# Kernel tuning notes

Hardware: AMD Instinct MI355X
Metric: run time of the kernel (lower is better)

Reference implementation:

```python
import jax, jax.numpy as jnp
import numpy as np

C = 768; H = 12; D = C // H; R = 8; SCALE = 0.5; EPS = 1e-12
NEG = -1e9

def _lin(x, W, b):
    return x @ W + b

def _ln(x, g, b):
    m = jnp.mean(x, axis=-1, keepdims=True)
    v = jnp.mean((x - m) ** 2, axis=-1, keepdims=True)
    return (x - m) * jax.lax.rsqrt(v + EPS) * g + b

def setup_inputs() -> dict:
    key = jax.random.key(0)
    ks = jax.random.split(key, 16)
    B, T, K = 8, 512, 4
    s = 0.02
    inp = {
        'x': jax.random.normal(ks[0], (B, T, C), jnp.float32),
        'mask': jnp.ones((B, T), jnp.int32),
        'neighbour_rep': jax.random.normal(ks[1], (B, T - 1, K, C), jnp.float32),
        'Wq': jax.random.normal(ks[2], (C, C), jnp.float32) * s,
        'bq': jnp.zeros((C,), jnp.float32),
        'Wk': jax.random.normal(ks[3], (C, C), jnp.float32) * s,
        'bk': jnp.zeros((C,), jnp.float32),
        'Wv': jax.random.normal(ks[4], (C, C), jnp.float32) * s,
        'bv': jnp.zeros((C,), jnp.float32),
        'Wp': jax.random.normal(ks[5], (C, C), jnp.float32) * s,
        'bp': jnp.zeros((C,), jnp.float32),
        'Wd': jax.random.normal(ks[6], (C, R), jnp.float32) * s,
        'bd': jnp.zeros((R,), jnp.float32),
        'Wu': jax.random.normal(ks[7], (R, C), jnp.float32) * s,
        'bu': jnp.zeros((C,), jnp.float32),
        'ln_g': jnp.ones((C,), jnp.float32),
        'ln_b': jnp.zeros((C,), jnp.float32),
    }
    return inp

def _softmax_stable(att):
    # manual max-sub-exp-sum softmax, matching stable_softmax
    att = att - jnp.max(att, axis=-1, keepdims=True)
    att = jnp.exp(att)
    return att / jnp.sum(att, axis=-1, keepdims=True)

def _heads(t, n_tok):
    B = t.shape[0]
    return t.reshape(B, n_tok, H, D)

def reference(x, mask, neighbour_rep, Wq, bq, Wk, bk, Wv, bv, Wp, bp, Wd, bd, Wu, bu, ln_g, ln_b):
    B, T, _ = x.shape
    inv = 1.0 / jnp.sqrt(jnp.float32(D))
    mvalid = (mask != 0)[:, None, None, :]  # [B,1,1,T]

    # ---- self attention: queries are x[:,1:], keys/values over full seq ----
    q = _heads(_lin(x[:, 1:], Wq, bq), T - 1)      # [B,T-1,H,D]
    k = _heads(_lin(x, Wk, bk), T)                 # [B,T,H,D]
    v = _heads(_lin(x, Wv, bv), T)
    att = jnp.einsum('bqhd,bkhd->bhqk', q, k) * inv
    att = jnp.where(mvalid, att, NEG)
    att = _softmax_stable(att)
    y_self = jnp.einsum('bhqk,bkhd->bqhd', att, v).reshape(B, T - 1, C)
    y_self = _lin(y_self, Wp, bp)

    # ---- cls attention: single query (token 0), low-rank key projection ----
    qc = _heads(_lin(x[:, :1], Wq, bq), 1)                         # [B,1,H,D]
    kc = _heads(_lin(_lin(x, Wd, bd), Wu, bu), T)                  # [B,T,H,D]
    attc = jnp.einsum('bqhd,bkhd->bhqk', qc, kc) * inv
    attc = jnp.where(mvalid, attc, NEG)
    attc = _softmax_stable(attc)
    y_cls = jnp.einsum('bhqk,bkhd->bqhd', attc, v).reshape(B, 1, C)
    y_cls = _lin(y_cls, Wp, bp)

    # ---- neighbour attention over small candidate set per token ----
    cand = jnp.concatenate([x[:, 1:, None, :], neighbour_rep], axis=2)  # [B,T-1,Kc,C]
    Kc = cand.shape[2]
    qn = _lin(cand, Wq, bq).reshape(B, T - 1, Kc, H, D)
    kn = _lin(_lin(cand, Wd, bd), Wu, bu).reshape(B, T - 1, Kc, H, D)
    vn = _lin(cand, Wv, bv).reshape(B, T - 1, Kc, H, D)
    attn = jnp.einsum('btihd,btjhd->bthij', qn, kn) * inv
    attn = _softmax_stable(attn)
    out = jnp.einsum('bthij,btjhd->btihd', attn, vn).reshape(B, T - 1, Kc, C)
    out = _lin(out, Wp, bp)
    y_neigh = out[:, :, 0, :]
    neigh_tmp = out[:, :, 1:, :]

    y = SCALE * y_neigh + (1.0 - SCALE) * y_self
    neighbour_out = _ln(neigh_tmp + neighbour_rep, ln_g, ln_b)
    y = jnp.concatenate([y_cls, y], axis=1)
    y = _ln(y + x, ln_g, ln_b)
    return y, neighbour_out
```

## Files before the change

kernel.cpp:

```cpp
#include <hip/hip_runtime.h>
#include <math.h>

#define C_    768
#define H_    12
#define D_    64
#define B_    8
#define T_    512
#define TM1   511
#define R_    8
#define KN_   4
#define KC5   5
#define SCALE_ 0.5f
#define EPS_  1e-12f
#define NEG_  -1000000000.0f
#define INV_  0.125f
#define LDQ   2560
#define QPOFF 2304
#define NT_   4096
#define NRR_  16352

typedef __bf16 bf16_t;
typedef __bf16 bf16x4_t __attribute__((ext_vector_type(4)));
typedef __bf16 bf16x8_t __attribute__((ext_vector_type(8)));
typedef float  f32x4_t  __attribute__((ext_vector_type(4)));
typedef const void __attribute__((address_space(1)))* gas_t;
typedef void       __attribute__((address_space(3)))* las_t;

__device__ __forceinline__ void gl_lds16(const bf16_t* g, bf16_t* l) {
  __builtin_amdgcn_global_load_lds((gas_t)g, (las_t)l, 16, 0, 0);
}

struct GemmDesc {
  const bf16_t* A; int lda;
  const bf16_t* Bt;
  const float* bias;
  bf16_t* Cbf; int ldc;
  bf16_t* Ctr; int trcol0; int mode;
  int M, K, N, gx, nwg;
};

__global__ __launch_bounds__(256) void prep(
    const float* __restrict__ x, const float* __restrict__ nrep,
    const float* __restrict__ Wq, const float* __restrict__ Wk,
    const float* __restrict__ Wv, const float* __restrict__ Wp,
    const float* __restrict__ Wd, const float* __restrict__ Wu,
    const float* __restrict__ bq, const float* __restrict__ bk,
    const float* __restrict__ bv, const float* __restrict__ bu,
    const float* __restrict__ bp,
    bf16_t* __restrict__ xbf, bf16_t* __restrict__ nrbf,
    bf16_t* __restrict__ Wbig, bf16_t* __restrict__ Wtp,
    bf16_t* __restrict__ Wvbf,
    float* __restrict__ WdT, float* __restrict__ bbig,
    float* __restrict__ zb768)
{
  __shared__ float tile[32][33];
  const int bid = blockIdx.x, tid = threadIdx.x;
  if (bid < 1024) {
    const long n = (long)NT_ * C_;
    for (long i = ((long)bid * 256 + tid) * 4; i < n; i += (long)1024 * 256 * 4) {
      float4 v = *(const float4*)(x + i);
      bf16x4_t o = {(bf16_t)v.x, (bf16_t)v.y, (bf16_t)v.z, (bf16_t)v.w};
      *(bf16x4_t*)(xbf + i) = o;
    }
  } else if (bid < 3072) {
    const long n = (long)NRR_ * C_;
    for (long i = ((long)(bid - 1024) * 256 + tid) * 4; i < n;
         i += (long)2048 * 256 * 4) {
      float4 v = *(const float4*)(nrep + i);
      bf16x4_t o = {(bf16_t)v.x, (bf16_t)v.y, (bf16_t)v.z, (bf16_t)v.w};
      *(bf16x4_t*)(nrbf + i) = o;
    }
  } else if (bid < 5376) {
    int sub = bid - 3072;
    const int which = sub / 576; sub %= 576;
    if (which == 2) {
      const long i = ((long)sub * 256 + tid) * 4;
      float4 v = *(const float4*)(Wv + i);
      bf16x4_t o = {(bf16_t)v.x, (bf16_t)v.y, (bf16_t)v.z, (bf16_t)v.w};
      *(bf16x4_t*)(Wvbf + i) = o;
    } else {
      const float* W = which == 0 ? Wq : which == 1 ? Wk : Wp;
      bf16_t* Wt = (which == 3) ? Wtp : Wbig + (size_t)which * C_ * C_;
      const int n0 = (sub % 24) * 32, k0 = (sub / 24) * 32;
      const int tx = tid & 31, ty = tid >> 5;
      #pragma unroll
      for (int r = ty; r < 32; r += 8)
        tile[r][tx] = W[(size_t)(k0 + r) * C_ + n0 + tx];
      __syncthreads();
      #pragma unroll
      for (int r = ty; r < 32; r += 8)
        Wt[(size_t)(n0 + r) * C_ + k0 + tx] = (bf16_t)tile[tx][r];
    }
  } else if (bid < 6144) {
    const int idx = (bid - 5376) * 256 + tid;
    const int n = idx / C_, k = idx % C_;
    const int h = n >> 4, r = n & 15;
    float s = 0.f;
    if (h < H_) {
      if (r < 8) {
        #pragma unroll 8
        for (int j = 0; j < 64; ++j)
          s += Wu[r * C_ + h * 64 + j] * Wq[(size_t)k * C_ + h * 64 + j];
      } else if (r == 8) {
        #pragma unroll 8
        for (int j = 0; j < 64; ++j)
          s += bu[h * 64 + j] * Wq[(size_t)k * C_ + h * 64 + j];
      }
    }
    Wbig[(size_t)(QPOFF + n) * C_ + k] = (bf16_t)s;
  } else if (bid < 6168) {
    const int idx = (bid - 6144) * 256 + tid;
    if (idx < R_ * C_) {
      const int r = idx / C_, k = idx % C_;
      WdT[idx] = Wd[(size_t)k * R_ + r];
    }
  } else {
    const int i = (bid - 6168) * 256 + tid;
    if (i < 2560) {
      float v;
      if (i < 768) v = bq[i];
      else if (i < 1536) v = bk[i - 768];
      else if (i < 2304) {
        const int n = i - 1536;
        float s = bp[n];
        for (int m = 0; m < C_; ++m) s += bv[m] * Wp[(size_t)m * C_ + n];
        v = s;
      } else {
        const int n = i - 2304, h = n >> 4, r = n & 15;
        v = 0.f;
        if (h < H_) {
          if (r < 8) {
            float s = 0.f;
            for (int j = 0; j < 64; ++j) s += bq[h * 64 + j] * Wu[r * C_ + h * 64 + j];
            v = s;
          } else if (r == 8) {
            float s = 0.f;
            for (int j = 0; j < 64; ++j) s += bq[h * 64 + j] * bu[h * 64 + j];
            v = s;
          }
        }
      }
      bbig[i] = v;
    } else if (i < 3328) {
      zb768[i - 2560] = 0.f;
    }
  }
}

__device__ __forceinline__ void gemm_body(const GemmDesc& d, int bid0, char* pool)
{
  bf16_t* As = (bf16_t*)pool;
  bf16_t* Bs = (bf16_t*)(pool + 16384);
  bf16_t* Cs = (bf16_t*)pool;

  int lid = bid0;
  {
    const int nwg = d.nwg;
    const int q0 = nwg >> 3, r0 = nwg & 7;
    const int xcd = lid & 7, idx = lid >> 3;
    lid = (xcd < r0 ? xcd * (q0 + 1) : r0 * (q0 + 1) + (xcd - r0) * q0) + idx;
  }
  const int row0 = (lid / d.gx) * 128;
  const int col0 = (lid % d.gx) * 128;

  const int tid = threadIdx.x;
  const int lane = tid & 63;
  const int wv = tid >> 6;
  const int wr = (wv >> 1) * 64;
  const int wc = (wv & 1) * 64;

  const int srl = wv * 8 + (lane >> 3);
  const int scol = 8 * ((lane & 7) ^ (srl & 7));

  const bf16_t* gA[4];
  const bf16_t* gB[4];
  #pragma unroll
  for (int i = 0; i < 4; ++i) {
    int ar = row0 + i * 32 + srl; if (ar > d.M - 1) ar = d.M - 1;
    gA[i] = d.A + (size_t)ar * d.lda + scol;
    gB[i] = d.Bt + (size_t)(col0 + i * 32 + srl) * d.K + scol;
  }

  f32x4_t acc[4][4];
  #pragma unroll
  for (int i = 0; i < 4; ++i)
    #pragma unroll
    for (int j = 0; j < 4; ++j) acc[i][j] = (f32x4_t){0.f, 0.f, 0.f, 0.f};

  const int fm = lane & 15;
  const int g = lane >> 4;
  const int f7 = fm & 7;

  for (int k0 = 0; k0 < d.K; k0 += 64) {
    #pragma unroll
    for (int i = 0; i < 4; ++i)
      gl_lds16(gA[i] + k0, As + i * 2048 + wv * 512);
    #pragma unroll
    for (int i = 0; i < 4; ++i)
      gl_lds16(gB[i] + k0, Bs + i * 2048 + wv * 512);
    __syncthreads();
    #pragma unroll
    for (int h = 0; h < 2; ++h) {
      const int sl = 8 * (((h << 2) + g) ^ f7);
      bf16x8_t af[4], bfr[4];
      #pragma unroll
      for (int mi = 0; mi < 4; ++mi)
        af[mi] = *(const bf16x8_t*)(As + (wr + mi * 16 + fm) * 64 + sl);
      #pragma unroll
      for (int ni = 0; ni < 4; ++ni)
        bfr[ni] = *(const bf16x8_t*)(Bs + (wc + ni * 16 + fm) * 64 + sl);
      __builtin_amdgcn_s_setprio(1);
      #pragma unroll
      for (int mi = 0; mi < 4; ++mi)
        #pragma unroll
        for (int ni = 0; ni < 4; ++ni)
          acc[mi][ni] = __builtin_amdgcn_mfma_f32_16x16x32_bf16(af[mi], bfr[ni],
                                                                acc[mi][ni], 0, 0, 0);
      __builtin_amdgcn_s_setprio(0);
    }
    __syncthreads();
  }

  const int r4 = (lane >> 4) * 4;

  if (d.mode & 2) {
    #pragma unroll
    for (int ni = 0; ni < 4; ++ni) {
      const int col = col0 + wc + ni * 16 + fm;
      if ((unsigned)(col - d.trcol0) < 768u) {
        const int vcol = col - d.trcol0;
        const float bv = d.bias[col];
        #pragma unroll
        for (int mi = 0; mi < 4; ++mi) {
          const int rb = row0 + wr + mi * 16 + r4;
          bf16x4_t o4 = {(bf16_t)(acc[mi][ni][0] + bv), (bf16_t)(acc[mi][ni][1] + bv),
                         (bf16_t)(acc[mi][ni][2] + bv), (bf16_t)(acc[mi][ni][3] + bv)};
          size_t idx = ((size_t)(rb >> 9) * H_ + (size_t)(vcol >> 6)) * ((size_t)D_ * T_)
                     + (size_t)(vcol & 63) * T_ + (size_t)(rb & 511);
          *(bf16x4_t*)(d.Ctr + idx) = o4;
        }
      }
    }
  }

  #pragma unroll
  for (int p = 0; p < 2; ++p) {
    if (wr == p * 64) {
      #pragma unroll
      for (int ni = 0; ni < 4; ++ni) {
        const int col = wc + ni * 16 + fm;
        const float bv = d.bias[col0 + col];
        #pragma unroll
        for (int mi = 0; mi < 4; ++mi) {
          const int lrow = mi * 16 + r4;
          #pragma unroll
          for (int r = 0; r < 4; ++r)
            Cs[(lrow + r) * 136 + col] = (bf16_t)(acc[mi][ni][r] + bv);
        }
      }
    }
    __syncthreads();
    const int rrow = tid >> 2;
    const int cc = (tid & 3) * 32;
    const int grow = row0 + p * 64 + rrow;
    if ((d.mode & 1) && grow < d.M) {
      bf16_t* gp = d.Cbf + (size_t)grow * d.ldc + col0 + cc;
      const bf16_t* lp = Cs + rrow * 136 + cc;
      #pragma unroll
      for (int j = 0; j < 4; ++j)
        *(bf16x8_t*)(gp + j * 8) = *(const bf16x8_t*)(lp + j * 8);
    }
    __syncthreads();
  }
}

__device__ __forceinline__ void gemv8w_body(
    const bf16_t* __restrict__ A, const float* __restrict__ WdT,
    const float* __restrict__ bd, float* __restrict__ out, int M, int bid)
{
  const int w = (int)threadIdx.x >> 6, lane = (int)threadIdx.x & 63;
  const int row0 = bid * 16 + w * 4;
  #pragma unroll
  for (int rr = 0; rr < 4; ++rr) {
    const int row = row0 + rr;
    if (row >= M) return;
    const bf16_t* ar = A + (size_t)row * C_ + lane * 12;
    float xv[12];
    #pragma unroll
    for (int c = 0; c < 3; ++c) {
      bf16x4_t v = *(const bf16x4_t*)(ar + c * 4);
      #pragma unroll
      for (int j = 0; j < 4; ++j) xv[c * 4 + j] = (float)v[j];
    }
    float acc[8];
    #pragma unroll
    for (int r = 0; r < 8; ++r) {
      const float* wr = WdT + r * C_ + lane * 12;
      float4 w0 = *(const float4*)(wr);
      float4 w1 = *(const float4*)(wr + 4);
      float4 w2 = *(const float4*)(wr + 8);
      acc[r] = xv[0]*w0.x + xv[1]*w0.y + xv[2]*w0.z + xv[3]*w0.w
             + xv[4]*w1.x + xv[5]*w1.y + xv[6]*w1.z + xv[7]*w1.w
             + xv[8]*w2.x + xv[9]*w2.y + xv[10]*w2.z + xv[11]*w2.w;
    }
    #pragma unroll
    for (int off = 32; off > 0; off >>= 1) {
      #pragma unroll
      for (int r = 0; r < 8; ++r) acc[r] += __shfl_xor(acc[r], off);
    }
    if (lane == 0) {
      #pragma unroll
      for (int r = 0; r < 8; ++r)
        out[(size_t)row * R_ + r] = acc[r] + bd[r];
    }
  }
}

__global__ __launch_bounds__(256) void mega1(
    GemmDesc d0, int n0, GemmDesc d1, int n1,
    const bf16_t* Ag1, const bf16_t* Ag2,
    const float* WdT, const float* bd,
    float* o1, int M1, int ng1, float* o2, int M2)
{
  __shared__ __align__(16) char pool[32768];
  int bid = blockIdx.x;
  if (bid < n0) { gemm_body(d0, bid, pool); return; }
  bid -= n0;
  if (bid < n1) { gemm_body(d1, bid, pool); return; }
  bid -= n1;
  if (bid < ng1) { gemv8w_body(Ag1, WdT, bd, o1, M1, bid); return; }
  bid -= ng1;
  gemv8w_body(Ag2, WdT, bd, o2, M2, bid);
}

__global__ __launch_bounds__(256) void gemm_mfma_k(GemmDesc d) {
  __shared__ __align__(16) char pool[32768];
  gemm_body(d, blockIdx.x, pool);
}

__device__ void attn_body(
    const bf16_t* __restrict__ QKVc, const bf16_t* __restrict__ Vtg,
    const int* __restrict__ mask, bf16_t* __restrict__ yout,
    char* pool, int bid)
{
  bf16_t* Ks   = (bf16_t*)pool;
  bf16_t* Vs   = (bf16_t*)(pool + 8192);
  bf16_t* Pl   = (bf16_t*)(pool + 16384);
  float* fac_s = (float*)(pool + 24576);
  float* l_s   = (float*)(pool + 24832);
  int*   msk_s = (int*)(pool + 25088);

  const int qt0 = (bid & 7) * 64;
  const int h = (bid >> 3) % H_;
  const int b = bid / 96;
  const int tid = threadIdx.x;
  const int lane = tid & 63;
  const int w = tid >> 6;
  const int lq = lane & 15;
  const int g = lane >> 4;

  const int qi_frag = qt0 + w * 16 + lq;
  const int qtok = (qi_frag < TM1 ? qi_frag : TM1 - 1) + 1;
  bf16x8_t qf[2];
  {
    const bf16_t* qp = QKVc + ((size_t)(b * T_) + qtok) * LDQ + h * D_ + 8 * g;
    qf[0] = *(const bf16x8_t*)qp;
    qf[1] = *(const bf16x8_t*)(qp + 32);
  }

  const bf16_t* kbase = QKVc + (size_t)(b * T_) * LDQ + 768 + h * D_;
  const bf16_t* vbase = Vtg + ((size_t)(b * H_) + h) * ((size_t)D_ * T_);

  f32x4_t o[4];
  #pragma unroll
  for (int i = 0; i < 4; ++i) o[i] = (f32x4_t){0.f, 0.f, 0.f, 0.f};
  float m = -INFINITY, l = 0.f;

  for (int kt = 0; kt < T_; kt += 64) {
    #pragma unroll
    for (int i = 0; i < 2; ++i) {
      const int tp = tid + i * 256;
      const int kr = tp >> 3;
      const int sl = tp & 7;
      const int ss = sl ^ (kr & 7);
      gl_lds16(kbase + (size_t)(kt + kr) * LDQ + 8 * ss,
               Ks + (size_t)(i * 4 + w) * 512);
      gl_lds16(vbase + (size_t)kr * T_ + kt + 8 * ss,
               Vs + (size_t)(i * 4 + w) * 512);
    }
    if (tid < 64) msk_s[tid] = mask[b * T_ + kt + tid];
    __syncthreads();

    f32x4_t st[4];
    __builtin_amdgcn_s_setprio(1);
    #pragma unroll
    for (int t = 0; t < 4; ++t) {
      st[t] = (f32x4_t){0.f, 0.f, 0.f, 0.f};
      const int kk = t * 16 + lq;
      const bf16_t* krow = Ks + kk * 64;
      bf16x8_t kf0 = *(const bf16x8_t*)(krow + 8 * ((g)     ^ (kk & 7)));
      bf16x8_t kf1 = *(const bf16x8_t*)(krow + 8 * ((4 + g) ^ (kk & 7)));
      st[t] = __builtin_amdgcn_mfma_f32_16x16x32_bf16(kf0, qf[0], st[t], 0, 0, 0);
      st[t] = __builtin_amdgcn_mfma_f32_16x16x32_bf16(kf1, qf[1], st[t], 0, 0, 0);
    }
    __builtin_amdgcn_s_setprio(0);

    float p[16];
    float mt = -INFINITY;
    #pragma unroll
    for (int t = 0; t < 4; ++t) {
      const int4 mk = *(const int4*)&msk_s[t * 16 + 4 * g];
      p[4*t+0] = mk.x ? st[t][0] * INV_ : NEG_;
      p[4*t+1] = mk.y ? st[t][1] * INV_ : NEG_;
      p[4*t+2] = mk.z ? st[t][2] * INV_ : NEG_;
      p[4*t+3] = mk.w ? st[t][3] * INV_ : NEG_;
      mt = fmaxf(mt, fmaxf(fmaxf(p[4*t], p[4*t+1]), fmaxf(p[4*t+2], p[4*t+3])));
    }
    mt = fmaxf(mt, __shfl_xor(mt, 16));
    mt = fmaxf(mt, __shfl_xor(mt, 32));
    const float mnew = fmaxf(m, mt);
    const float fac = __expf(m - mnew);
    float ps = 0.f;
    #pragma unroll
    for (int i = 0; i < 16; ++i) { p[i] = __expf(p[i] - mnew); ps += p[i]; }
    ps += __shfl_xor(ps, 16);
    ps += __shfl_xor(ps, 32);
    l = l * fac + ps;
    m = mnew;
    if (lane < 16) fac_s[w * 16 + lane] = fac;

    bf16_t* prow = Pl + w * 1024 + lq * 64;
    #pragma unroll
    for (int t = 0; t < 4; ++t) {
      bf16x4_t pb = {(bf16_t)p[4*t], (bf16_t)p[4*t+1],
                     (bf16_t)p[4*t+2], (bf16_t)p[4*t+3]};
      *(bf16x4_t*)(prow + 8 * ((2*t + (g >> 1)) ^ (lq & 7)) + 4 * (g & 1)) = pb;
    }
    bf16x8_t pa0 = *(const bf16x8_t*)(prow + 8 * ((g)     ^ (lq & 7)));
    bf16x8_t pa1 = *(const bf16x8_t*)(prow + 8 * ((4 + g) ^ (lq & 7)));

    const float4 fc = *(const float4*)&fac_s[w * 16 + 4 * g];
    __builtin_amdgcn_s_setprio(1);
    #pragma unroll
    for (int db = 0; db < 4; ++db) {
      const int dr = db * 16 + lq;
      const bf16_t* vrow = Vs + dr * 64;
      bf16x8_t vf0 = *(const bf16x8_t*)(vrow + 8 * ((g)     ^ (dr & 7)));
      bf16x8_t vf1 = *(const bf16x8_t*)(vrow + 8 * ((4 + g) ^ (dr & 7)));
      o[db][0] *= fc.x; o[db][1] *= fc.y; o[db][2] *= fc.z; o[db][3] *= fc.w;
      o[db] = __builtin_amdgcn_mfma_f32_16x16x32_bf16(pa0, vf0, o[db], 0, 0, 0);
      o[db] = __builtin_amdgcn_mfma_f32_16x16x32_bf16(pa1, vf1, o[db], 0, 0, 0);
    }
    __builtin_amdgcn_s_setprio(0);
    __syncthreads();
  }

  if (lane < 16) l_s[w * 16 + lane] = l;
  const float4 lv = *(const float4*)&l_s[w * 16 + 4 * g];
  const float rl0 = 1.f / lv.x, rl1 = 1.f / lv.y;
  const float rl2 = 1.f / lv.z, rl3 = 1.f / lv.w;
  const int qr0 = qt0 + w * 16 + 4 * g;
  #pragma unroll
  for (int db = 0; db < 4; ++db) {
    const int col = h * D_ + db * 16 + lq;
    bf16_t* yp = yout + ((size_t)(b * TM1) + qr0) * C_ + col;
    if (qr0 + 0 < TM1) yp[0 * (size_t)C_] = (bf16_t)(o[db][0] * rl0);
    if (qr0 + 1 < TM1) yp[1 * (size_t)C_] = (bf16_t)(o[db][1] * rl1);
    if (qr0 + 2 < TM1) yp[2 * (size_t)C_] = (bf16_t)(o[db][2] * rl2);
    if (qr0 + 3 < TM1) yp[3 * (size_t)C_] = (bf16_t)(o[db][3] * rl3);
  }
}

__device__ void cls_body(
    const bf16_t* __restrict__ QKVc, const float* __restrict__ t1,
    const int* __restrict__ mask, float* __restrict__ ycp,
    char* pool, int cbid)
{
  float* Vs   = (float*)pool;
  float* Ps   = (float*)(pool + 16640);
  float* qp_s = (float*)(pool + 16960);

  const int b = cbid / H_, h = cbid % H_;
  const int tid = threadIdx.x;
  const int lane = tid & 63;

  if (tid < 16)
    qp_s[tid] = (float)QKVc[(size_t)(b * T_) * LDQ + QPOFF + h * 16 + tid];
  __syncthreads();

  float m = -INFINITY, l = 0.f, acc = 0.f, mnew = 0.f;
  for (int kt = 0; kt < T_; kt += 64) {
    for (int rr = tid >> 6; rr < 64; rr += 4)
      Vs[rr * 65 + lane] =
          (float)QKVc[((size_t)(b * T_) + kt + rr) * LDQ + 1536 + h * D_ + lane];
    __syncthreads();
    if (tid < 64) {
      const float* t1r = t1 + ((size_t)(b * T_) + kt + tid) * R_;
      float sc = qp_s[8];
      #pragma unroll
      for (int r = 0; r < 8; ++r) sc += qp_s[r] * t1r[r];
      sc *= INV_;
      if (!mask[b * T_ + kt + tid]) sc = NEG_;
      float mt = sc;
      #pragma unroll
      for (int off = 32; off > 0; off >>= 1) mt = fmaxf(mt, __shfl_xor(mt, off));
      mnew = fmaxf(m, mt);
      float e = __expf(sc - mnew);
      float ssum = e;
      #pragma unroll
      for (int off = 32; off > 0; off >>= 1) ssum += __shfl_xor(ssum, off);
      float fac = __expf(m - mnew);
      acc *= fac;
      l = l * fac + ssum;
      Ps[tid] = e;
    }
    __syncthreads();
    if (tid < 64) {
      #pragma unroll
      for (int j = 0; j < 64; ++j) acc += Ps[j] * Vs[j * 65 + tid];
      m = mnew;
    }
    __syncthreads();
  }
  if (tid < 64) ycp[(size_t)b * C_ + h * D_ + tid] = acc / l;
}

__global__ __launch_bounds__(256) void attn_cls(
    const bf16_t* __restrict__ QKVc, const bf16_t* __restrict__ Vtg,
    const int* __restrict__ mask, bf16_t* __restrict__ yout,
    const float* __restrict__ t1, float* __restrict__ ycp)
{
  __shared__ __align__(16) char pool[25344];
  const int bid = blockIdx.x;
  if (bid < 768) attn_body(QKVc, Vtg, mask, yout, pool, bid);
  else           cls_body(QKVc, t1, mask, ycp, pool, bid - 768);
}

__global__ __launch_bounds__(256) void neigh_attn(
    const bf16_t* __restrict__ QKVc, const float* __restrict__ t1,
    const bf16_t* __restrict__ vqn, const float* __restrict__ t2,
    const bf16_t* __restrict__ ysp, int b0, bf16_t* __restrict__ poutn)
{
  __shared__ float vs[KC5 * C_];
  __shared__ float qp_s[KC5][200];
  __shared__ float t2_s[KC5][8];
  __shared__ float Ps[H_ * 25];

  const int tid = threadIdx.x;
  const int bt = blockIdx.x;
  const int bb = bt / TM1, t = bt % TM1;
  const int b = b0 + bb;
  const size_t tok = (size_t)(b * T_) + t + 1;
  const size_t nrow = ((size_t)(bb * TM1) + t) * KN_;

  for (int idx = tid; idx < KC5 * 96; idx += 256) {
    int i = idx / 96, d8 = (idx % 96) * 8;
    const bf16_t* vp = (i == 0) ? QKVc + tok * LDQ + 1536 + d8
                                : vqn + (nrow + i - 1) * 1024 + d8;
    bf16x8_t vv = *(const bf16x8_t*)vp;
    #pragma unroll
    for (int j = 0; j < 8; ++j) vs[i * C_ + d8 + j] = (float)vv[j];
  }
  for (int idx = tid; idx < KC5 * 24; idx += 256) {
    int i = idx / 24, c8 = (idx % 24) * 8;
    const bf16_t* qpp = (i == 0) ? QKVc + tok * LDQ + QPOFF + c8
                                 : vqn + (nrow + i - 1) * 1024 + 768 + c8;
    bf16x8_t qv = *(const bf16x8_t*)qpp;
    #pragma unroll
    for (int j = 0; j < 8; ++j) qp_s[i][c8 + j] = (float)qv[j];
  }
  if (tid < KC5 * 8) {
    int i = tid / 8, r = tid & 7;
    t2_s[i][r] = (i == 0) ? t1[tok * R_ + r] : t2[(nrow + i - 1) * R_ + r];
  }
  __syncthreads();

  if (tid < H_ * KC5) {
    int h = tid / KC5, i = tid % KC5;
    float sc[KC5];
    #pragma unroll
    for (int j = 0; j < KC5; ++j) {
      float s = qp_s[i][h * 16 + 8];
      #pragma unroll
      for (int r = 0; r < 8; ++r) s += qp_s[i][h * 16 + r] * t2_s[j][r];
      sc[j] = s * INV_;
    }
    float mt = sc[0];
    #pragma unroll
    for (int j = 1; j < KC5; ++j) mt = fmaxf(mt, sc[j]);
    float e[KC5], ssum = 0.f;
    #pragma unroll
    for (int j = 0; j < KC5; ++j) { e[j] = __expf(sc[j] - mt); ssum += e[j]; }
    float rs = 1.f / ssum;
    #pragma unroll
    for (int j = 0; j < KC5; ++j) Ps[h * 25 + i * KC5 + j] = e[j] * rs;
  }
  __syncthreads();

  const bf16_t* ysrow = ysp + ((size_t)(b * TM1) + t) * C_;
  for (int idx = tid; idx < KC5 * C_; idx += 256) {
    int i = idx / C_, c = idx % C_;
    int h = c / D_;
    float sum = 0.f;
    #pragma unroll
    for (int j = 0; j < KC5; ++j)
      sum += Ps[h * 25 + i * KC5 + j] * vs[j * C_ + c];
    if (i == 0) sum = SCALE_ * sum + (1.f - SCALE_) * (float)ysrow[c];
    poutn[(((size_t)(bb * TM1) + t) * KC5 + i) * C_ + c] = (bf16_t)sum;
  }
}

__device__ __forceinline__ void block_reduce2(float& s, float& ss, float* red) {
  #pragma unroll
  for (int off = 32; off > 0; off >>= 1) {
    s += __shfl_down(s, off);
    ss += __shfl_down(ss, off);
  }
  int wid = threadIdx.x >> 6;
  if ((threadIdx.x & 63) == 0) { red[wid * 2] = s; red[wid * 2 + 1] = ss; }
  __syncthreads();
  s  = red[0] + red[2] + red[4] + red[6];
  ss = red[1] + red[3] + red[5] + red[7];
}

__device__ __forceinline__ void ln_row(const float vals[3], float s, float ss,
                                       const float* __restrict__ g,
                                       const float* __restrict__ bb,
                                       float* __restrict__ orow, float* red) {
  block_reduce2(s, ss, red);
  float mean = s * (1.f / (float)C_);
  float var = ss * (1.f / (float)C_) - mean * mean;
  var = fmaxf(var, 0.f);
  float rs = rsqrtf(var + EPS_);
  #pragma unroll
  for (int ii = 0; ii < 3; ++ii) {
    int c = threadIdx.x + ii * 256;
    orow[c] = (vals[ii] - mean) * rs * g[c] + bb[c];
  }
}

__global__ __launch_bounds__(256) void combine_all(
    const bf16_t* __restrict__ poutnb, const float* __restrict__ x,
    const float* __restrict__ g, const float* __restrict__ bln,
    int b0, float* __restrict__ dout, float* __restrict__ dout1,
    const bf16_t* __restrict__ nrcbf, int nMain,
    const float* __restrict__ ycp, int withCls)
{
  __shared__ float red[8];
  int bid = blockIdx.x;
  float vals[3], s = 0.f, ss = 0.f;
  if (bid < nMain) {
    const int bbb = bid / TM1, t = bid % TM1;
    const int b = b0 + bbb;
    const bf16_t* pn = poutnb + (((size_t)(bbb * TM1) + t) * KC5 + 0) * C_;
    const float* xr = x + ((size_t)(b * T_) + t + 1) * C_;
    float* orow = dout + ((size_t)(b * T_) + t + 1) * C_;
    #pragma unroll
    for (int ii = 0; ii < 3; ++ii) {
      int c = threadIdx.x + ii * 256;
      float v = (float)pn[c] + xr[c];
      vals[ii] = v; s += v; ss += v * v;
    }
    ln_row(vals, s, ss, g, bln, orow, red);
    return;
  }
  bid -= nMain;
  if (bid < nMain * KN_) {
    const int i1 = bid % KN_;
    const int bt = bid / KN_;
    const int bbb = bt / TM1, t = bt % TM1;
    const int b = b0 + bbb;
    const bf16_t* pn = poutnb + ((size_t)bt * KC5 + 1 + i1) * C_;
    const bf16_t* nr = nrcbf + ((size_t)bt * KN_ + i1) * C_;
    float* orow = dout1 + (((size_t)(b * TM1) + t) * KN_ + i1) * C_;
    #pragma unroll
    for (int ii = 0; ii < 3; ++ii) {
      int c = threadIdx.x + ii * 256;
      float v = (float)pn[c] + (float)nr[c];
      vals[ii] = v; s += v; ss += v * v;
    }
    ln_row(vals, s, ss, g, bln, orow, red);
    return;
  }
  bid -= nMain * KN_;
  (void)withCls;
  const int b = bid;
  const float* yc = ycp + (size_t)b * C_;
  const float* xr = x + (size_t)(b * T_) * C_;
  float* orow = dout + (size_t)(b * T_) * C_;
  #pragma unroll
  for (int ii = 0; ii < 3; ++ii) {
    int c = threadIdx.x + ii * 256;
    float v = yc[c] + xr[c];
    vals[ii] = v; s += v; ss += v * v;
  }
  ln_row(vals, s, ss, g, bln, orow, red);
}

extern "C" void kernel_launch(void* const* d_in, const int* in_sizes, int n_in,
                              void* d_out, int out_size, void* d_ws, size_t ws_size,
                              hipStream_t stream) {
  (void)in_sizes; (void)n_in; (void)out_size;
  const float* x    = (const float*)d_in[0];
  const int*   mask = (const int*)d_in[1];
  const float* nrep = (const float*)d_in[2];
  const float* Wq = (const float*)d_in[3];  const float* bq = (const float*)d_in[4];
  const float* Wk = (const float*)d_in[5];  const float* bk = (const float*)d_in[6];
  const float* Wv = (const float*)d_in[7];  const float* bv = (const float*)d_in[8];
  const float* Wp = (const float*)d_in[9];  const float* bp = (const float*)d_in[10];
  const float* Wd = (const float*)d_in[11]; const float* bd = (const float*)d_in[12];
  const float* Wu = (const float*)d_in[13]; const float* bu = (const float*)d_in[14];
  const float* lng = (const float*)d_in[15];
  const float* lnb = (const float*)d_in[16];
  float* dout = (float*)d_out;
  const size_t OUT1 = (size_t)B_ * T_ * C_;

  char* ws = (char*)d_ws;
  size_t off = 0;
  auto alloc = [&](size_t bytes) -> void* {
    void* p = ws + off; off += (bytes + 255) & ~(size_t)255; return p;
  };
  const size_t NT = (size_t)NT_;
  const size_t NR = (size_t)NRR_;
  const size_t YSROWS = (size_t)B_ * TM1;

  bf16_t* xbf   = (bf16_t*)alloc(NT * C_ * 2);
  bf16_t* nrbf  = (bf16_t*)alloc(NR * C_ * 2);
  bf16_t* Wbig  = (bf16_t*)alloc((size_t)2560 * C_ * 2);
  bf16_t* Wtp   = (bf16_t*)alloc((size_t)C_ * C_ * 2);
  bf16_t* Wvbf  = (bf16_t*)alloc((size_t)C_ * C_ * 2);
  float*  WdT   = (float*)alloc((size_t)R_ * C_ * 4);
  float*  bbig  = (float*)alloc(2560 * 4);
  float*  zb768 = (float*)alloc(768 * 4);
  bf16_t* QKVc  = (bf16_t*)alloc(NT * LDQ * 2);
  bf16_t* Vtg   = (bf16_t*)alloc(NT * C_ * 2);
  float*  t1    = (float*)alloc(NT * R_ * 4);
  bf16_t* ysp   = (bf16_t*)alloc(YSROWS * C_ * 2);
  float*  ycp   = (float*)alloc((size_t)B_ * C_ * 4);
  const size_t fixed = off;
  const size_t perb = (size_t)TM1 * KN_ * 1024 * 2
                    + (size_t)TM1 * KN_ * R_ * 4
                    + (size_t)TM1 * KC5 * C_ * 2 + 4 * 256;
  int nb = 1;
  for (int cand : {8, 4, 2, 1}) {
    if (fixed + perb * (size_t)cand <= ws_size) { nb = cand; break; }
  }
  bf16_t* poutnb = (bf16_t*)alloc((size_t)nb * TM1 * KC5 * C_ * 2);
  bf16_t* vqn  = (bf16_t*)alloc((size_t)nb * TM1 * KN_ * 1024 * 2);
  float*  t2   = (float*)alloc((size_t)nb * TM1 * KN_ * R_ * 4);

  dim3 blk(256);

  prep<<<6181, blk, 0, stream>>>(x, nrep, Wq, Wk, Wv, Wp, Wd, Wu,
                                 bq, bk, bv, bu, bp,
                                 xbf, nrbf, Wbig, Wtp, Wvbf, WdT, bbig, zb768);

  GemmDesc dwvp;
  dwvp.A = Wtp; dwvp.lda = C_; dwvp.Bt = Wvbf; dwvp.bias = zb768;
  dwvp.Cbf = Wbig + (size_t)1536 * C_; dwvp.ldc = C_;
  dwvp.Ctr = nullptr; dwvp.trcol0 = 0; dwvp.mode = 1;
  dwvp.M = C_; dwvp.K = C_; dwvp.N = C_; dwvp.gx = 6; dwvp.nwg = 36;
  gemm_mfma_k<<<36, blk, 0, stream>>>(dwvp);

  GemmDesc dqkv;
  dqkv.A = xbf; dqkv.lda = C_; dqkv.Bt = Wbig; dqkv.bias = bbig;
  dqkv.Cbf = QKVc; dqkv.ldc = LDQ; dqkv.Ctr = Vtg; dqkv.trcol0 = 1536;
  dqkv.mode = 3; dqkv.M = (int)NT; dqkv.K = C_; dqkv.N = 2560;
  dqkv.gx = 20; dqkv.nwg = 640;

  bool first = true;
  for (int b0 = 0; b0 < B_; b0 += nb) {
    const int Mn = nb * TM1 * KN_;
    const bf16_t* nrcbf = nrbf + (size_t)b0 * TM1 * KN_ * C_;

    GemmDesc dvqn;
    dvqn.A = nrcbf; dvqn.lda = C_; dvqn.Bt = Wbig + (size_t)1536 * C_;
    dvqn.bias = bbig + 1536; dvqn.Cbf = vqn; dvqn.ldc = 1024;
    dvqn.Ctr = nullptr; dvqn.trcol0 = 0; dvqn.mode = 1;
    dvqn.M = Mn; dvqn.K = C_; dvqn.N = 1024;
    dvqn.gx = 8; dvqn.nwg = 8 * ((Mn + 127) / 128);

    const int n0 = first ? 640 : 0;
    const int M1 = first ? (int)NT : 0;
    const int ng1 = first ? (int)((NT + 15) / 16) : 0;
    const int ng2 = (Mn + 15) / 16;

    mega1<<<n0 + dvqn.nwg + ng1 + ng2, blk, 0, stream>>>(
        dqkv, n0, dvqn, dvqn.nwg, xbf, nrcbf, WdT, bd, t1, M1, ng1, t2, Mn);

    if (first) {
      attn_cls<<<768 + 96, blk, 0, stream>>>(QKVc, Vtg, mask, ysp, t1, ycp);
    }

    neigh_attn<<<nb * TM1, blk, 0, stream>>>(QKVc, t1, vqn, t2, ysp, b0, poutnb);

    combine_all<<<nb * TM1 * (1 + KN_) + (first ? 8 : 0), blk, 0, stream>>>(
        poutnb, x, lng, lnb, b0, dout, dout + OUT1, nrcbf, nb * TM1,
        ycp, first ? 1 : 0);

    first = false;
  }
}
```

Measured before the change: 242.7 us.

## Move neighbour V/Q GEMM into attention launch and defer self-attn mixing to combine

The neighbour V/Q projection GEMM moves out of the first fused launch and into a new fused kernel alongside self-attention and cls attention. The aim is to balance work across the two launches so the GEMM blocks can fill the GPU while the attention blocks run. The blend of self-attention output with the neighbour output moves from neigh_attn into combine_all, so neigh_attn no longer depends on ysp. The cost is that the mega_b shared pool grows to 32KB, which may lower attention occupancy, and combine_all reads an extra bf16 row.

```diff
diff --git a/kernel.cpp b/kernel.cpp
--- a/kernel.cpp
+++ b/kernel.cpp
@@ -316,8 +316,8 @@
   }
 }
 
-__global__ __launch_bounds__(256) void mega1(
-    GemmDesc d0, int n0, GemmDesc d1, int n1,
+__global__ __launch_bounds__(256) void mega_a(
+    GemmDesc d0, int n0,
     const bf16_t* Ag1, const bf16_t* Ag2,
     const float* WdT, const float* bd,
     float* o1, int M1, int ng1, float* o2, int M2)
@@ -326,8 +326,6 @@
   int bid = blockIdx.x;
   if (bid < n0) { gemm_body(d0, bid, pool); return; }
   bid -= n0;
-  if (bid < n1) { gemm_body(d1, bid, pool); return; }
-  bid -= n1;
   if (bid < ng1) { gemv8w_body(Ag1, WdT, bd, o1, M1, bid); return; }
   bid -= ng1;
   gemv8w_body(Ag2, WdT, bd, o2, M2, bid);
@@ -525,21 +523,25 @@
   if (tid < 64) ycp[(size_t)b * C_ + h * D_ + tid] = acc / l;
 }
 
-__global__ __launch_bounds__(256) void attn_cls(
+__global__ __launch_bounds__(256) void mega_b(
+    GemmDesc d1, int n1, int nAttn,
     const bf16_t* __restrict__ QKVc, const bf16_t* __restrict__ Vtg,
-    const int* __restrict__ mask, bf16_t* __restrict__ yout,
+    const int* __restrict__ mask, bf16_t* __restrict__ ysp,
     const float* __restrict__ t1, float* __restrict__ ycp)
 {
-  __shared__ __align__(16) char pool[25344];
-  const int bid = blockIdx.x;
-  if (bid < 768) attn_body(QKVc, Vtg, mask, yout, pool, bid);
-  else           cls_body(QKVc, t1, mask, ycp, pool, bid - 768);
+  __shared__ __align__(16) char pool[32768];
+  int bid = blockIdx.x;
+  if (bid < n1) { gemm_body(d1, bid, pool); return; }
+  bid -= n1;
+  if (bid < nAttn) { attn_body(QKVc, Vtg, mask, ysp, pool, bid); return; }
+  bid -= nAttn;
+  cls_body(QKVc, t1, mask, ycp, pool, bid);
 }
 
 __global__ __launch_bounds__(256) void neigh_attn(
     const bf16_t* __restrict__ QKVc, const float* __restrict__ t1,
     const bf16_t* __restrict__ vqn, const float* __restrict__ t2,
-    const bf16_t* __restrict__ ysp, int b0, bf16_t* __restrict__ poutn)
+    int b0, bf16_t* __restrict__ poutn)
 {
   __shared__ float vs[KC5 * C_];
   __shared__ float qp_s[KC5][200];
@@ -597,7 +599,6 @@
   }
   __syncthreads();
 
-  const bf16_t* ysrow = ysp + ((size_t)(b * TM1) + t) * C_;
   for (int idx = tid; idx < KC5 * C_; idx += 256) {
     int i = idx / C_, c = idx % C_;
     int h = c / D_;
@@ -605,7 +606,6 @@
     #pragma unroll
     for (int j = 0; j < KC5; ++j)
       sum += Ps[h * 25 + i * KC5 + j] * vs[j * C_ + c];
-    if (i == 0) sum = SCALE_ * sum + (1.f - SCALE_) * (float)ysrow[c];
     poutn[(((size_t)(bb * TM1) + t) * KC5 + i) * C_ + c] = (bf16_t)sum;
   }
 }
@@ -640,11 +640,12 @@
 }
 
 __global__ __launch_bounds__(256) void combine_all(
-    const bf16_t* __restrict__ poutnb, const float* __restrict__ x,
+    const bf16_t* __restrict__ poutnb, const bf16_t* __restrict__ ysp,
+    const float* __restrict__ x,
     const float* __restrict__ g, const float* __restrict__ bln,
     int b0, float* __restrict__ dout, float* __restrict__ dout1,
     const bf16_t* __restrict__ nrcbf, int nMain,
-    const float* __restrict__ ycp, int withCls)
+    const float* __restrict__ ycp)
 {
   __shared__ float red[8];
   int bid = blockIdx.x;
@@ -653,12 +654,13 @@
     const int bbb = bid / TM1, t = bid % TM1;
     const int b = b0 + bbb;
     const bf16_t* pn = poutnb + (((size_t)(bbb * TM1) + t) * KC5 + 0) * C_;
+    const bf16_t* ys = ysp + ((size_t)(b * TM1) + t) * C_;
     const float* xr = x + ((size_t)(b * T_) + t + 1) * C_;
     float* orow = dout + ((size_t)(b * T_) + t + 1) * C_;
     #pragma unroll
     for (int ii = 0; ii < 3; ++ii) {
       int c = threadIdx.x + ii * 256;
-      float v = (float)pn[c] + xr[c];
+      float v = SCALE_ * (float)pn[c] + (1.f - SCALE_) * (float)ys[c] + xr[c];
       vals[ii] = v; s += v; ss += v * v;
     }
     ln_row(vals, s, ss, g, bln, orow, red);
@@ -683,7 +685,6 @@
     return;
   }
   bid -= nMain * KN_;
-  (void)withCls;
   const int b = bid;
   const float* yc = ycp + (size_t)b * C_;
   const float* xr = x + (size_t)(b * T_) * C_;
@@ -785,18 +786,18 @@
     const int ng1 = first ? (int)((NT + 15) / 16) : 0;
     const int ng2 = (Mn + 15) / 16;
 
-    mega1<<<n0 + dvqn.nwg + ng1 + ng2, blk, 0, stream>>>(
-        dqkv, n0, dvqn, dvqn.nwg, xbf, nrcbf, WdT, bd, t1, M1, ng1, t2, Mn);
-
-    if (first) {
-      attn_cls<<<768 + 96, blk, 0, stream>>>(QKVc, Vtg, mask, ysp, t1, ycp);
-    }
-
-    neigh_attn<<<nb * TM1, blk, 0, stream>>>(QKVc, t1, vqn, t2, ysp, b0, poutnb);
+    mega_a<<<n0 + ng1 + ng2, blk, 0, stream>>>(
+        dqkv, n0, xbf, nrcbf, WdT, bd, t1, M1, ng1, t2, Mn);
+
+    const int nAttn = first ? 768 : 0;
+    const int nCls  = first ? 96 : 0;
+    mega_b<<<dvqn.nwg + nAttn + nCls, blk, 0, stream>>>(
+        dvqn, dvqn.nwg, nAttn, QKVc, Vtg, mask, ysp, t1, ycp);
+
+    neigh_attn<<<nb * TM1, blk, 0, stream>>>(QKVc, t1, vqn, t2, b0, poutnb);
 
     combine_all<<<nb * TM1 * (1 + KN_) + (first ? 8 : 0), blk, 0, stream>>>(
-        poutnb, x, lng, lnb, b0, dout, dout + OUT1, nrcbf, nb * TM1,
-        ycp, first ? 1 : 0);
+        poutnb, ysp, x, lng, lnb, b0, dout, dout + OUT1, nrcbf, nb * TM1, ycp);
 
     first = false;
   }
```

New measurement: 250.9 us. 1.03x slower.
